# Kernel optimization log

Measured on AMD Instinct MI355X. Metric: run time of the kernel, lower is better.

## Reference

```python
import jax, jax.numpy as jnp
import numpy as np

B, C, H, W = 8, 19, 512, 512
FOCAL_GAMMA = 2.0
LABEL_SMOOTH = 0.1
DICE_SMOOTH = 1e-05
BOUNDARY_W = 0.5  # BoundaryLoss internal boundary_weight
W_FOCAL = W_DICE = W_CE = W_BOUNDARY = 1.0  # config term weights


def setup_inputs() -> dict:
    key = jax.random.key(0)
    k1, k2 = jax.random.split(key)
    inputs = jax.random.normal(k1, (B, C, H, W), dtype=jnp.float32)
    targets = jax.random.randint(k2, (B, H, W), 0, C, dtype=jnp.int32)
    return {"inputs": inputs, "targets": targets}


def _boundary_map(t):
    # Faithful to the torch loops: patch.max(dim=1)-patch.min(dim=1) reduces over the
    # 3 ROW offsets per column; then .any() collapses batch AND the 3 columns,
    # and the flag is written for ALL batch elements.
    vmax = jnp.maximum(jnp.maximum(t[:, :-2, :], t[:, 1:-1, :]), t[:, 2:, :])  # [B,H-2,W]
    vmin = jnp.minimum(jnp.minimum(t[:, :-2, :], t[:, 1:-1, :]), t[:, 2:, :])
    diff = jnp.any(vmax != vmin, axis=0)                                       # [H-2,W] any over batch
    hb = diff[:, :-2] | diff[:, 1:-1] | diff[:, 2:]                            # [H-2,W-2] any over 3 cols
    bm = jnp.zeros((t.shape[1], t.shape[2]), jnp.float32).at[1:-1, 1:-1].set(hb.astype(jnp.float32))
    return jnp.broadcast_to(bm[None], t.shape)                                 # [B,H,W]


def _combined(inputs, targets):
    lp = jax.nn.log_softmax(inputs, axis=1)                                    # [B,C,H,W]
    lp_t = jnp.take_along_axis(lp, targets[:, None].astype(jnp.int32), axis=1)[:, 0]  # [B,H,W]
    nll = -lp_t

    # Focal (alpha=None, no ignored pixels present)
    p_t = jnp.exp(lp_t)
    focal = jnp.mean((1.0 - p_t) ** FOCAL_GAMMA * nll)

    # Dice over all classes (vectorized over class dim)
    probs = jnp.exp(lp)
    onehot = (targets[:, None, :, :] == jnp.arange(C, dtype=targets.dtype)[None, :, None, None])
    onehot = onehot.astype(inputs.dtype)
    inter = jnp.einsum('bchw,bchw->c', probs, onehot)
    denom = jnp.sum(probs, axis=(0, 2, 3)) + jnp.sum(onehot, axis=(0, 2, 3))
    dice = jnp.mean(1.0 - (2.0 * inter + DICE_SMOOTH) / (denom + DICE_SMOOTH))

    # CE with label smoothing 0.1 (torch formula)
    smooth_term = -jnp.mean(lp, axis=1)  # (1/C) * sum_c -log p_c, [B,H,W]
    ce = jnp.mean((1.0 - LABEL_SMOOTH) * nll + LABEL_SMOOTH * smooth_term)

    # Boundary-weighted CE
    bmap = _boundary_map(targets)
    boundary = jnp.mean(nll * (1.0 + BOUNDARY_W * bmap))

    total = W_FOCAL * focal + W_DICE * dice + W_CE * ce + W_BOUNDARY * boundary
    return jnp.stack([focal, dice, ce, boundary, total])


def reference(inputs, targets):
    return _combined(inputs, targets)
```

## Files before the change

kernel.cpp:

```cpp
#include <hip/hip_runtime.h>

#define H_ 512
#define W_ 512
#define B_ 8
#define C_ 19
#define HW_ (H_ * W_)
#define NPIX (B_ * HW_)
#define NGROUPS (NPIX / 4)

#define MAIN_BLOCKS 512
#define MAIN_THREADS 256
#define PSTRIDE 64
#define DIFF_ELEMS ((H_ - 2) * W_)
#define DIFF_BYTES_PAD 262144

#define NVALS 61

__device__ __forceinline__ float wred(float v) {
    v += __shfl_down(v, 32);
    v += __shfl_down(v, 16);
    v += __shfl_down(v, 8);
    v += __shfl_down(v, 4);
    v += __shfl_down(v, 2);
    v += __shfl_down(v, 1);
    return v;
}

__global__ void diff_kernel(const int* __restrict__ tgt, unsigned char* __restrict__ diff) {
    int idx = blockIdx.x * blockDim.x + threadIdx.x;
    if (idx >= DIFF_ELEMS) return;
    int flag = 0;
    const int* p = tgt + idx;
#pragma unroll
    for (int b = 0; b < B_; ++b) {
        int t0 = p[0];
        int t1 = p[W_];
        int t2 = p[2 * W_];
        flag |= (int)(t0 != t1) | (int)(t1 != t2);
        p += HW_;
    }
    diff[idx] = (unsigned char)flag;
}

__global__ __launch_bounds__(MAIN_THREADS, 2) void main_kernel(
    const float* __restrict__ x, const int* __restrict__ tgt,
    const unsigned char* __restrict__ diff, float* __restrict__ partials)
{
    float acc[NVALS];
#pragma unroll
    for (int k = 0; k < NVALS; ++k) acc[k] = 0.f;

    const int tid = threadIdx.x;
    const int stride = MAIN_BLOCKS * MAIN_THREADS;

    for (int g = blockIdx.x * MAIN_THREADS + tid; g < NGROUPS; g += stride) {
        const int p0 = g << 2;
        const int b  = p0 >> 18;
        const int hw = p0 & (HW_ - 1);
        const int h  = hw >> 9;
        const int w0 = hw & (W_ - 1);

        const float4* xp = (const float4*)(x + (size_t)b * (C_ * HW_) + hw);
        float v[C_][4];
#pragma unroll
        for (int c = 0; c < C_; ++c) {
            float4 t = xp[c * (HW_ / 4)];
            v[c][0] = t.x; v[c][1] = t.y; v[c][2] = t.z; v[c][3] = t.w;
        }
        const int4 t4 = ((const int4*)tgt)[g];
        const int tArr[4] = {t4.x, t4.y, t4.z, t4.w};

        const bool hOK = (h >= 1) && (h <= H_ - 2);
        const int drow = (h - 1) << 9;

#pragma unroll
        for (int i = 0; i < 4; ++i) {
            const int t = tArr[i];
            float m = v[0][i];
#pragma unroll
            for (int c = 1; c < C_; ++c) m = fmaxf(m, v[c][i]);
            float se = 0.f, sx = 0.f, xt = 0.f, et = 0.f;
#pragma unroll
            for (int c = 0; c < C_; ++c) {
                const float xv = v[c][i];
                const float e = __expf(xv - m);
                se += e;
                sx += xv;
                const bool sel = (c == t);
                xt = sel ? xv : xt;
                et = sel ? e : et;
                v[c][i] = e;
            }
            const float invse = 1.f / se;
            const float lsum = __logf(se);
            const float nll = lsum - (xt - m);
            const float pt = et * invse;
            const float omp = 1.f - pt;
            acc[0] += omp * omp * nll;
            acc[1] += nll;
            acc[2] += (lsum + m) - sx * (1.f / C_);
            const int w = w0 + i;
            float bf = 0.f;
            if (hOK && w >= 1 && w <= W_ - 2) {
                const int dbase = drow + (w - 1);
                const unsigned d = (unsigned)diff[dbase] | (unsigned)diff[dbase + 1]
                                 | (unsigned)diff[dbase + 2];
                bf = d ? 1.f : 0.f;
            }
            acc[3] += nll * bf;
#pragma unroll
            for (int c = 0; c < C_; ++c) {
                acc[4 + c] += v[c][i] * invse;
                const bool sel = (c == t);
                acc[23 + c] += sel ? pt : 0.f;
                acc[42 + c] += sel ? 1.f : 0.f;
            }
        }
    }

    __shared__ float red[MAIN_THREADS / 64][NVALS];
    const int lane = tid & 63;
    const int wid = tid >> 6;
#pragma unroll
    for (int k = 0; k < NVALS; ++k) {
        const float r = wred(acc[k]);
        if (lane == 0) red[wid][k] = r;
    }
    __syncthreads();
    if (tid < NVALS) {
        float s = 0.f;
#pragma unroll
        for (int wv = 0; wv < MAIN_THREADS / 64; ++wv) s += red[wv][tid];
        partials[blockIdx.x * PSTRIDE + tid] = s;
    }
}

__global__ void finalize_kernel(const float* __restrict__ partials, float* __restrict__ out) {
    __shared__ double grp[4][NVALS];
    const int tid = threadIdx.x;
    const int lane = tid & 63;
    const int g = tid >> 6;
    if (lane < NVALS) {
        double s = 0.0;
        for (int b = g; b < MAIN_BLOCKS; b += 4)
            s += (double)partials[b * PSTRIDE + lane];
        grp[g][lane] = s;
    }
    __syncthreads();
    if (tid == 0) {
        double sums[NVALS];
        for (int k = 0; k < NVALS; ++k)
            sums[k] = grp[0][k] + grp[1][k] + grp[2][k] + grp[3][k];
        const double Np = (double)NPIX;
        const double focal = sums[0] / Np;
        const double ce = (0.9 * sums[1] + 0.1 * sums[2]) / Np;
        const double boundary = (sums[1] + 0.5 * sums[3]) / Np;
        double dice = 0.0;
        for (int c = 0; c < C_; ++c) {
            const double I2 = 2.0 * sums[23 + c] + 1e-5;
            const double D = sums[4 + c] + sums[42 + c] + 1e-5;
            dice += 1.0 - I2 / D;
        }
        dice /= (double)C_;
        const double total = focal + dice + ce + boundary;
        out[0] = (float)focal;
        out[1] = (float)dice;
        out[2] = (float)ce;
        out[3] = (float)boundary;
        out[4] = (float)total;
    }
}

extern "C" void kernel_launch(void* const* d_in, const int* in_sizes, int n_in,
                              void* d_out, int out_size, void* d_ws, size_t ws_size,
                              hipStream_t stream) {
    const float* x = (const float*)d_in[0];
    const int* tgt = (const int*)d_in[1];
    float* out = (float*)d_out;
    unsigned char* diff = (unsigned char*)d_ws;
    float* partials = (float*)((char*)d_ws + DIFF_BYTES_PAD);

    diff_kernel<<<(DIFF_ELEMS + 255) / 256, 256, 0, stream>>>(tgt, diff);
    main_kernel<<<MAIN_BLOCKS, MAIN_THREADS, 0, stream>>>(x, tgt, diff, partials);
    finalize_kernel<<<1, 256, 0, stream>>>(partials, out);
}
```

Baseline: 276.9 us.

## Accumulate per-class dice terms via shared atomics, raise occupancy, use nontemporal loads

Replaces the 38 per-thread one-hot accumulators for intersection and counts with shared-memory atomic adds indexed by the target class. This cuts register pressure and per-pixel select work, which allows launch bounds to request 3 blocks per CU instead of 2. Input logits are now read with nontemporal loads to avoid polluting cache. The cost is LDS atomic contention on a small set of class bins, and float atomics make the summation order nondeterministic.

```diff
diff --git a/kernel.cpp b/kernel.cpp
--- a/kernel.cpp
+++ b/kernel.cpp
@@ -14,7 +14,10 @@
 #define DIFF_ELEMS ((H_ - 2) * W_)
 #define DIFF_BYTES_PAD 262144
 
+#define NDENSE 23
 #define NVALS 61
+
+typedef float vf4 __attribute__((ext_vector_type(4)));
 
 __device__ __forceinline__ float wred(float v) {
     v += __shfl_down(v, 32);
@@ -42,15 +45,20 @@
     diff[idx] = (unsigned char)flag;
 }
 
-__global__ __launch_bounds__(MAIN_THREADS, 2) void main_kernel(
+__global__ __launch_bounds__(MAIN_THREADS, 3) void main_kernel(
     const float* __restrict__ x, const int* __restrict__ tgt,
     const unsigned char* __restrict__ diff, float* __restrict__ partials)
 {
-    float acc[NVALS];
+    __shared__ float s_inter[C_];
+    __shared__ unsigned s_cnt[C_];
+    const int tid = threadIdx.x;
+    if (tid < C_) { s_inter[tid] = 0.f; s_cnt[tid] = 0u; }
+    __syncthreads();
+
+    float acc[NDENSE];
 #pragma unroll
-    for (int k = 0; k < NVALS; ++k) acc[k] = 0.f;
+    for (int k = 0; k < NDENSE; ++k) acc[k] = 0.f;
 
-    const int tid = threadIdx.x;
     const int stride = MAIN_BLOCKS * MAIN_THREADS;
 
     for (int g = blockIdx.x * MAIN_THREADS + tid; g < NGROUPS; g += stride) {
@@ -60,11 +68,11 @@
         const int h  = hw >> 9;
         const int w0 = hw & (W_ - 1);
 
-        const float4* xp = (const float4*)(x + (size_t)b * (C_ * HW_) + hw);
+        const vf4* xp = (const vf4*)(x + (size_t)b * (C_ * HW_) + hw);
         float v[C_][4];
 #pragma unroll
         for (int c = 0; c < C_; ++c) {
-            float4 t = xp[c * (HW_ / 4)];
+            vf4 t = __builtin_nontemporal_load(xp + c * (HW_ / 4));
             v[c][0] = t.x; v[c][1] = t.y; v[c][2] = t.z; v[c][3] = t.w;
         }
         const int4 t4 = ((const int4*)tgt)[g];
@@ -109,29 +117,33 @@
             }
             acc[3] += nll * bf;
 #pragma unroll
-            for (int c = 0; c < C_; ++c) {
+            for (int c = 0; c < C_; ++c)
                 acc[4 + c] += v[c][i] * invse;
-                const bool sel = (c == t);
-                acc[23 + c] += sel ? pt : 0.f;
-                acc[42 + c] += sel ? 1.f : 0.f;
-            }
+            atomicAdd(&s_inter[t], pt);
+            atomicAdd(&s_cnt[t], 1u);
         }
     }
 
-    __shared__ float red[MAIN_THREADS / 64][NVALS];
+    __shared__ float red[MAIN_THREADS / 64][NDENSE];
     const int lane = tid & 63;
     const int wid = tid >> 6;
 #pragma unroll
-    for (int k = 0; k < NVALS; ++k) {
+    for (int k = 0; k < NDENSE; ++k) {
         const float r = wred(acc[k]);
         if (lane == 0) red[wid][k] = r;
     }
     __syncthreads();
-    if (tid < NVALS) {
+    float* rec = partials + blockIdx.x * PSTRIDE;
+    if (tid < NDENSE) {
         float s = 0.f;
 #pragma unroll
         for (int wv = 0; wv < MAIN_THREADS / 64; ++wv) s += red[wv][tid];
-        partials[blockIdx.x * PSTRIDE + tid] = s;
+        rec[tid] = s;
+    }
+    if (tid >= 64 && tid < 64 + C_) {
+        const int c = tid - 64;
+        rec[23 + c] = s_inter[c];
+        rec[42 + c] = (float)s_cnt[c];
     }
 }
 
```

New measurement: 281.3 us. About the same (+1.6%).
